# Kernel tuning notes

Hardware: AMD Instinct MI355X
Metric: run time of the kernel (lower is better)

Reference implementation:

```python
import jax, jax.numpy as jnp
import numpy as np

E = 1024
H = 16
D = E // H  # head_dim = 64
FF = 4 * E
EPS = 1e-5


def layernorm(x, g, b):
    mu = jnp.mean(x, axis=-1, keepdims=True)
    var = jnp.var(x, axis=-1, keepdims=True)
    return (x - mu) * jax.lax.rsqrt(var + EPS) * g + b


def setup_inputs() -> dict:
    key = jax.random.key(0)
    ks = jax.random.split(key, 12)
    s = 1.0 / np.sqrt(E)
    sf = 1.0 / np.sqrt(FF)
    return {
        "x": jax.random.normal(ks[0], (2, 2048, E), dtype=jnp.float32),
        "wq": jax.random.uniform(ks[1], (E, E), jnp.float32, -s, s),
        "wk": jax.random.uniform(ks[2], (E, E), jnp.float32, -s, s),
        "wv": jax.random.uniform(ks[3], (E, E), jnp.float32, -s, s),
        "wo": jax.random.uniform(ks[4], (E, E), jnp.float32, -s, s),
        "bo": jax.random.uniform(ks[5], (E,), jnp.float32, -s, s),
        "g1": jnp.ones((E,), jnp.float32),
        "b1": jnp.zeros((E,), jnp.float32),
        "w1": jax.random.uniform(ks[6], (FF, E), jnp.float32, -s, s),
        "bf1": jax.random.uniform(ks[7], (FF,), jnp.float32, -s, s),
        "w2": jax.random.uniform(ks[8], (E, FF), jnp.float32, -sf, sf),
        "bf2": jax.random.uniform(ks[9], (E,), jnp.float32, -sf, sf),
        "g2": jnp.ones((E,), jnp.float32),
        "b2": jnp.zeros((E,), jnp.float32),
    }


def reference(x, wq, wk, wv, wo, bo, g1, b1, w1, bf1, w2, bf2, g2, b2):
    B, L, _ = x.shape
    # projections (torch Linear: x @ W.T)
    q = (x @ wq.T).reshape(B, L, H, D).transpose(0, 2, 1, 3)  # (B,H,L,D)
    k = (x @ wk.T).reshape(B, L, H, D).transpose(0, 2, 1, 3)
    v = (x @ wv.T).reshape(B, L, H, D).transpose(0, 2, 1, 3)
    scores = jnp.einsum('bhqd,bhkd->bhqk', q, k) / np.sqrt(D)
    attn = jax.nn.softmax(scores, axis=-1)
    ctx = jnp.einsum('bhqk,bhkd->bhqd', attn, v)
    ctx = ctx.transpose(0, 2, 1, 3).reshape(B, L, E)
    attn_out = ctx @ wo.T + bo
    h = layernorm(x + attn_out, g1, b1)
    ff = jax.nn.gelu(h @ w1.T + bf1, approximate=False) @ w2.T + bf2
    return layernorm(h + ff, g2, b2)
```

## Files before the change

kernel.cpp:

```cpp
#include <hip/hip_runtime.h>
#include <hip/hip_bf16.h>
#include <stdint.h>

typedef __bf16 bf16x8 __attribute__((ext_vector_type(8)));
typedef float  f32x4  __attribute__((ext_vector_type(4)));
typedef unsigned short u16;
typedef u16 u16x8 __attribute__((ext_vector_type(8)));

__device__ __forceinline__ u16 f2b(float f) {
  uint32_t u = __builtin_bit_cast(uint32_t, f);
  u += 0x7fffu + ((u >> 16) & 1u);
  return (u16)(u >> 16);
}

__device__ __forceinline__ f32x4 mfma16(bf16x8 a, bf16x8 b, f32x4 c) {
  return __builtin_amdgcn_mfma_f32_16x16x32_bf16(a, b, c, 0, 0, 0);
}

__device__ __forceinline__ void gload_lds16(const void* g, void* l) {
  __builtin_amdgcn_global_load_lds(
      (const __attribute__((address_space(1))) void*)g,
      (__attribute__((address_space(3))) void*)l, 16, 0, 0);
}

__global__ void f2b_all(const float* __restrict__ x,  const float* __restrict__ wq,
                        const float* __restrict__ wk, const float* __restrict__ wv,
                        const float* __restrict__ wo, const float* __restrict__ w1,
                        const float* __restrict__ w2,
                        u16* __restrict__ xb, u16* __restrict__ wqkvb,
                        u16* __restrict__ wob, u16* __restrict__ w1b,
                        u16* __restrict__ w2b) {
  const int i = blockIdx.x * blockDim.x + threadIdx.x;
  const float* src; u16* dst; int off;
  if (i < 524288)        { src = x;  dst = xb;              off = i; }
  else if (i < 655360)   { src = wq; dst = wqkvb;           off = i - 524288; }
  else if (i < 786432)   { src = wk; dst = wqkvb + 1048576; off = i - 655360; }
  else if (i < 917504)   { src = wv; dst = wqkvb + 2097152; off = i - 786432; }
  else if (i < 1048576)  { src = wo; dst = wob;             off = i - 917504; }
  else if (i < 1572864)  { src = w1; dst = w1b;             off = i - 1048576; }
  else                   { src = w2; dst = w2b;             off = i - 1572864; }
  const float4* p = (const float4*)src + (size_t)off * 2;
  float4 a = p[0], b = p[1];
  u16x8 r;
  r[0] = f2b(a.x); r[1] = f2b(a.y); r[2] = f2b(a.z); r[3] = f2b(a.w);
  r[4] = f2b(b.x); r[5] = f2b(b.y); r[6] = f2b(b.z); r[7] = f2b(b.w);
  *((u16x8*)dst + off) = r;
}

template<int MODE>
__global__ __launch_bounds__(256, 3) void gemm_bt(
    const u16* __restrict__ A, const u16* __restrict__ W,
    const float* __restrict__ bias,
    void* __restrict__ o0, void* __restrict__ o1, void* __restrict__ o2,
    int Nsz, int Kstride, int Klen, int ntiles)
{
  __shared__ u16 As[2][128 * 32];
  __shared__ u16 Bs[2][128 * 32];
  const int nbn = Nsz >> 7;
  int bid = blockIdx.x;
  bid = (bid & 7) * ((int)gridDim.x >> 3) + (bid >> 3);
  const int tile = (MODE == 1) ? (bid % ntiles) : bid;
  const int sid  = (MODE == 1) ? (bid / ntiles) : 0;
  const int koff = sid * Klen;
  const int bm = tile / nbn;
  const int bn = tile % nbn;
  const int tid = threadIdx.x;
  const int w = tid >> 6, l = tid & 63;
  const int lh = l >> 4, ll = l & 15;
  const int wr = w >> 1, wc = w & 1;

  f32x4 acc[4][4] = {};

  const u16* Ag = A + (size_t)(bm * 128) * Kstride + koff;
  const u16* Wg = W + (size_t)(bn * 128) * Kstride + koff;

  const int flat0 = (w * 2) * 64 + l;
  const int flat1 = (w * 2 + 1) * 64 + l;

  {
    gload_lds16(Ag + (size_t)(flat0 >> 2) * Kstride + (flat0 & 3) * 8, As[0] + flat0 * 8);
    gload_lds16(Wg + (size_t)(flat0 >> 2) * Kstride + (flat0 & 3) * 8, Bs[0] + flat0 * 8);
    gload_lds16(Ag + (size_t)(flat1 >> 2) * Kstride + (flat1 & 3) * 8, As[0] + flat1 * 8);
    gload_lds16(Wg + (size_t)(flat1 >> 2) * Kstride + (flat1 & 3) * 8, Bs[0] + flat1 * 8);
  }
  __syncthreads();

  const int NS = Klen >> 5;
  int buf = 0;
  for (int s = 0; s < NS; ++s) {
    if (s + 1 < NS) {
      const int k0 = (s + 1) * 32;
      gload_lds16(Ag + (size_t)(flat0 >> 2) * Kstride + k0 + (flat0 & 3) * 8, As[buf ^ 1] + flat0 * 8);
      gload_lds16(Wg + (size_t)(flat0 >> 2) * Kstride + k0 + (flat0 & 3) * 8, Bs[buf ^ 1] + flat0 * 8);
      gload_lds16(Ag + (size_t)(flat1 >> 2) * Kstride + k0 + (flat1 & 3) * 8, As[buf ^ 1] + flat1 * 8);
      gload_lds16(Wg + (size_t)(flat1 >> 2) * Kstride + k0 + (flat1 & 3) * 8, Bs[buf ^ 1] + flat1 * 8);
    }
    bf16x8 af[4], bfr[4];
#pragma unroll
    for (int mi = 0; mi < 4; ++mi)
      af[mi] = *(const bf16x8*)(As[buf] + (wr * 64 + mi * 16 + ll) * 32 + lh * 8);
#pragma unroll
    for (int ni = 0; ni < 4; ++ni)
      bfr[ni] = *(const bf16x8*)(Bs[buf] + (wc * 64 + ni * 16 + ll) * 32 + lh * 8);
    __builtin_amdgcn_s_setprio(1);
#pragma unroll
    for (int mi = 0; mi < 4; ++mi)
#pragma unroll
      for (int ni = 0; ni < 4; ++ni)
        acc[mi][ni] = mfma16(af[mi], bfr[ni], acc[mi][ni]);
    __builtin_amdgcn_s_setprio(0);
    __syncthreads();
    buf ^= 1;
  }

#pragma unroll
  for (int mi = 0; mi < 4; ++mi) {
#pragma unroll
    for (int ni = 0; ni < 4; ++ni) {
      const int col = bn * 128 + wc * 64 + ni * 16 + ll;
#pragma unroll
      for (int i = 0; i < 4; ++i) {
        const int row = bm * 128 + wr * 64 + mi * 16 + lh * 4 + i;
        float v = acc[mi][ni][i];
        if (MODE == 1) {
          float* dst = sid ? (float*)o1 : (float*)o0;
          dst[(size_t)row * Nsz + col] = v;
        } else if (MODE == 2) {
          float xx = v + bias[col];
          float gl = 0.5f * xx * (1.0f + erff(xx * 0.70710678118654752f));
          ((u16*)o0)[(size_t)row * Nsz + col] = f2b(gl);
        } else {
          const int which = col >> 10;
          const int e = col & 1023;
          const int hh = e >> 6, dd = e & 63;
          const int bb = row >> 11, nl = row & 2047;
          if (which == 0) {
            ((u16*)o0)[((size_t)(bb * 16 + hh) * 2048 + nl) * 64 + dd] = f2b(v * 0.18033688f);
          } else if (which == 1) {
            ((u16*)o1)[((size_t)(bb * 16 + hh) * 2048 + nl) * 64 + dd] = f2b(v);
          } else {
            ((u16*)o2)[((size_t)(bb * 16 + hh) * 64 + dd) * 2048 + nl] = f2b(v);
          }
        }
      }
    }
  }
}

__global__ __launch_bounds__(256, 4) void attn_fwd(
    const u16* __restrict__ Q, const u16* __restrict__ K,
    const u16* __restrict__ Vt, u16* __restrict__ ctx)
{
  __shared__ u16 Ks[2][64 * 64];
  __shared__ u16 Vs[2][64 * 64];
  __shared__ u16 Ps[4][16 * 64];

  const int bh = blockIdx.x & 31;
  const int qt = blockIdx.x >> 5;
  const int tid = threadIdx.x;
  const int w = tid >> 6, l = tid & 63;
  const int lh = l >> 4, ll = l & 15;
  const int q0 = qt * 64 + w * 16;

  bf16x8 qf[2];
  {
    const u16* Qg = Q + ((size_t)bh * 2048 + q0 + ll) * 64;
#pragma unroll
    for (int kk = 0; kk < 2; ++kk)
      qf[kk] = *(const bf16x8*)(Qg + kk * 32 + lh * 8);
  }

  bf16x8 ones;
  {
    const u16 o = 0x3F80;
#pragma unroll
    for (int i = 0; i < 8; ++i) ones[i] = __builtin_bit_cast(__bf16, o);
  }

  f32x4 cacc[4] = {};
  f32x4 lacc = {};
  float m_l = -1e30f;
  u16* ps = Ps[w];

  const int f0 = tid, f1 = 256 + tid;
  const int r0 = f0 >> 3, s0 = f0 & 7, g0 = (s0 ^ (r0 & 7)) * 8;
  const int r1 = f1 >> 3, s1 = f1 & 7, g1 = (s1 ^ (r1 & 7)) * 8;

  {
    gload_lds16(K + ((size_t)bh * 2048 + r0) * 64 + g0, Ks[0] + f0 * 8);
    gload_lds16(Vt + ((size_t)bh * 64 + r0) * 2048 + g0, Vs[0] + f0 * 8);
    gload_lds16(K + ((size_t)bh * 2048 + r1) * 64 + g1, Ks[0] + f1 * 8);
    gload_lds16(Vt + ((size_t)bh * 64 + r1) * 2048 + g1, Vs[0] + f1 * 8);
  }
  __syncthreads();

  for (int kt = 0; kt < 32; ++kt) {
    const int b = kt & 1;
    if (kt < 31) {
      const int kn = (kt + 1) * 64;
      gload_lds16(K + ((size_t)bh * 2048 + kn + r0) * 64 + g0, Ks[b ^ 1] + f0 * 8);
      gload_lds16(Vt + ((size_t)bh * 64 + r0) * 2048 + kn + g0, Vs[b ^ 1] + f0 * 8);
      gload_lds16(K + ((size_t)bh * 2048 + kn + r1) * 64 + g1, Ks[b ^ 1] + f1 * 8);
      gload_lds16(Vt + ((size_t)bh * 64 + r1) * 2048 + kn + g1, Vs[b ^ 1] + f1 * 8);
    }

    f32x4 st[4];
    __builtin_amdgcn_s_setprio(1);
#pragma unroll
    for (int jb = 0; jb < 4; ++jb) {
      f32x4 a = {};
#pragma unroll
      for (int kk = 0; kk < 2; ++kk) {
        const int r = jb * 16 + ll;
        bf16x8 kf = *(const bf16x8*)(Ks[b] + r * 64 + (((kk * 4 + lh) ^ (r & 7)) * 8));
        a = mfma16(kf, qf[kk], a);
      }
      st[jb] = a;
    }
    __builtin_amdgcn_s_setprio(0);

    float mx = fmaxf(fmaxf(fmaxf(st[0][0], st[0][1]), fmaxf(st[0][2], st[0][3])),
                     fmaxf(fmaxf(st[1][0], st[1][1]), fmaxf(st[1][2], st[1][3])));
    mx = fmaxf(mx, fmaxf(fmaxf(fmaxf(st[2][0], st[2][1]), fmaxf(st[2][2], st[2][3])),
                         fmaxf(fmaxf(st[3][0], st[3][1]), fmaxf(st[3][2], st[3][3]))));
    mx = fmaxf(mx, __shfl_xor(mx, 16));
    mx = fmaxf(mx, __shfl_xor(mx, 32));

    if (!__all(mx - m_l <= 8.0f)) {
      const float mn = fmaxf(m_l, mx);
      const float al = __builtin_amdgcn_exp2f(m_l - mn);
      m_l = mn;
      float alq[4];
#pragma unroll
      for (int i = 0; i < 4; ++i) alq[i] = __shfl(al, lh * 4 + i);
#pragma unroll
      for (int db = 0; db < 4; ++db)
#pragma unroll
        for (int i = 0; i < 4; ++i) cacc[db][i] *= alq[i];
#pragma unroll
      for (int i = 0; i < 4; ++i) lacc[i] *= alq[i];
    }

#pragma unroll
    for (int jb = 0; jb < 4; ++jb) {
      const float p0 = __builtin_amdgcn_exp2f(st[jb][0] - m_l);
      const float p1 = __builtin_amdgcn_exp2f(st[jb][1] - m_l);
      const float p2 = __builtin_amdgcn_exp2f(st[jb][2] - m_l);
      const float p3 = __builtin_amdgcn_exp2f(st[jb][3] - m_l);
      uint2 pk;
      asm("v_cvt_pk_bf16_f32 %0, %1, %2" : "=v"(pk.x) : "v"(p0), "v"(p1));
      asm("v_cvt_pk_bf16_f32 %0, %1, %2" : "=v"(pk.y) : "v"(p2), "v"(p3));
      *(uint2*)(ps + ll * 64 + (((jb * 2 + (lh >> 1)) ^ (ll & 7)) * 8) + (lh & 1) * 4) = pk;
    }

    asm volatile("s_waitcnt lgkmcnt(0)" ::: "memory");
    __builtin_amdgcn_sched_barrier(0);

    __builtin_amdgcn_s_setprio(1);
#pragma unroll
    for (int kk = 0; kk < 2; ++kk) {
      bf16x8 pf = *(const bf16x8*)(ps + ll * 64 + (((kk * 4 + lh) ^ (ll & 7)) * 8));
      lacc = mfma16(pf, ones, lacc);
#pragma unroll
      for (int db = 0; db < 4; ++db) {
        const int vr = db * 16 + ll;
        bf16x8 vf = *(const bf16x8*)(Vs[b] + vr * 64 + (((kk * 4 + lh) ^ (vr & 7)) * 8));
        cacc[db] = mfma16(pf, vf, cacc[db]);
      }
    }
    __builtin_amdgcn_s_setprio(0);
    __syncthreads();
  }

  const int bb = bh >> 4, hh = bh & 15;
#pragma unroll
  for (int db = 0; db < 4; ++db)
#pragma unroll
    for (int i = 0; i < 4; ++i) {
      const float v = cacc[db][i] / lacc[i];
      const size_t orow = (size_t)bb * 2048 + q0 + lh * 4 + i;
      const size_t ocol = (size_t)hh * 64 + db * 16 + ll;
      ctx[orow * 1024 + ocol] = f2b(v);
    }
}

__global__ __launch_bounds__(256) void ln_fused(
    const float* __restrict__ a,  const float* __restrict__ b0,
    const float* __restrict__ b1, const float* __restrict__ b2,
    const float* __restrict__ b3, const float* __restrict__ bias,
    const float* __restrict__ g,  const float* __restrict__ be,
    float* __restrict__ ho, u16* __restrict__ hb)
{
  const int row = blockIdx.x;
  const int t = threadIdx.x;
  const size_t base = (size_t)row * 1024 + t * 4;
  float4 xa = *(const float4*)(a + base);
  float4 xb = *(const float4*)(b0 + base);
  float v0 = xa.x + xb.x, v1 = xa.y + xb.y, v2 = xa.z + xb.z, v3 = xa.w + xb.w;
  if (b1) {
    float4 xc = *(const float4*)(b1 + base);
    v0 += xc.x; v1 += xc.y; v2 += xc.z; v3 += xc.w;
  }
  if (b2) {
    float4 xc = *(const float4*)(b2 + base);
    v0 += xc.x; v1 += xc.y; v2 += xc.z; v3 += xc.w;
  }
  if (b3) {
    float4 xc = *(const float4*)(b3 + base);
    v0 += xc.x; v1 += xc.y; v2 += xc.z; v3 += xc.w;
  }
  if (bias) {
    float4 xd = *(const float4*)(bias + t * 4);
    v0 += xd.x; v1 += xd.y; v2 += xd.z; v3 += xd.w;
  }
  float s = v0 + v1 + v2 + v3;
  float ss = v0 * v0 + v1 * v1 + v2 * v2 + v3 * v3;
#pragma unroll
  for (int d = 1; d < 64; d <<= 1) {
    s += __shfl_xor(s, d);
    ss += __shfl_xor(ss, d);
  }
  __shared__ float red[8];
  const int w = t >> 6, lid = t & 63;
  if (lid == 0) { red[w] = s; red[4 + w] = ss; }
  __syncthreads();
  s = red[0] + red[1] + red[2] + red[3];
  ss = red[4] + red[5] + red[6] + red[7];
  const float mean = s * (1.0f / 1024.0f);
  const float var = ss * (1.0f / 1024.0f) - mean * mean;
  const float rstd = rsqrtf(var + 1e-5f);
  const float vv[4] = {v0, v1, v2, v3};
#pragma unroll
  for (int i = 0; i < 4; ++i) {
    const int col = t * 4 + i;
    const float hv = (vv[i] - mean) * rstd * g[col] + be[col];
    if (ho) ho[base + i] = hv;
    if (hb) hb[base + i] = f2b(hv);
  }
}

extern "C" void kernel_launch(void* const* d_in, const int* in_sizes, int n_in,
                              void* d_out, int out_size, void* d_ws, size_t ws_size,
                              hipStream_t stream) {
  const float* x   = (const float*)d_in[0];
  const float* wq  = (const float*)d_in[1];
  const float* wk  = (const float*)d_in[2];
  const float* wv  = (const float*)d_in[3];
  const float* wo  = (const float*)d_in[4];
  const float* bo  = (const float*)d_in[5];
  const float* g1  = (const float*)d_in[6];
  const float* b1  = (const float*)d_in[7];
  const float* w1  = (const float*)d_in[8];
  const float* bf1 = (const float*)d_in[9];
  const float* w2  = (const float*)d_in[10];
  const float* bf2 = (const float*)d_in[11];
  const float* g2  = (const float*)d_in[12];
  const float* b2  = (const float*)d_in[13];

  char* ws = (char*)d_ws;
  const size_t MB = 1u << 20;
  u16* xb    = (u16*)(ws + 0);
  u16* wqkv  = (u16*)(ws + 8 * MB);
  u16* wob   = (u16*)(ws + 14 * MB);
  u16* w1b   = (u16*)(ws + 16 * MB);
  u16* w2b   = (u16*)(ws + 24 * MB);
  u16* qb    = (u16*)(ws + 32 * MB);
  u16* kb    = (u16*)(ws + 40 * MB);
  u16* vtb   = (u16*)(ws + 48 * MB);
  u16* ctxb  = (u16*)(ws + 56 * MB);
  float* pA   = (float*)(ws + 64 * MB);
  float* hbuf = (float*)(ws + 80 * MB);
  u16* hbb   = (u16*)(ws + 96 * MB);
  float* wo_p1 = (float*)(ws + 32 * MB);
  u16* ff1   = (u16*)(ws + 32 * MB);
  float* f2_p1 = (float*)(ws + 0);

  f2b_all<<<8192, 256, 0, stream>>>(x, wq, wk, wv, wo, w1, w2, xb, wqkv, wob, w1b, w2b);

  gemm_bt<0><<<768, 256, 0, stream>>>(xb, wqkv, nullptr, qb, kb, vtb, 3072, 1024, 1024, 768);
  attn_fwd<<<1024, 256, 0, stream>>>(qb, kb, vtb, ctxb);
  gemm_bt<1><<<512, 256, 0, stream>>>(ctxb, wob, nullptr, pA, wo_p1, nullptr, 1024, 1024, 512, 256);
  ln_fused<<<4096, 256, 0, stream>>>(x, pA, wo_p1, nullptr, nullptr, bo, g1, b1, hbuf, hbb);
  gemm_bt<2><<<1024, 256, 0, stream>>>(hbb, w1b, bf1, ff1, nullptr, nullptr, 4096, 1024, 1024, 1024);
  gemm_bt<1><<<512, 256, 0, stream>>>(ff1, w2b, nullptr, pA, f2_p1, nullptr, 1024, 4096, 2048, 256);
  ln_fused<<<4096, 256, 0, stream>>>(hbuf, pA, f2_p1, nullptr, nullptr, bf2, g2, b2,
                                     (float*)d_out, nullptr);
}
```

Before: 267.9 us.

## Process two query tiles per wave in attention and use tanh-form GELU

The attention kernel now handles 32 query rows per wave (128 per block), so each K and V tile loaded into shared memory feeds twice as many MFMAs. This halves the grid and the redundant K/V traffic, at the cost of more registers, hence the occupancy hint drops from 4 to 3. The FFN1 epilogue also replaces the exact erf GELU with the tanh approximation, computed via exp2 and a reciprocal. That approximation deviates from the reference's exact GELU.

```diff
diff --git a/kernel.cpp b/kernel.cpp
--- a/kernel.cpp
+++ b/kernel.cpp
@@ -127,8 +127,10 @@
           dst[(size_t)row * Nsz + col] = v;
         } else if (MODE == 2) {
           float xx = v + bias[col];
-          float gl = 0.5f * xx * (1.0f + erff(xx * 0.70710678118654752f));
-          ((u16*)o0)[(size_t)row * Nsz + col] = f2b(gl);
+          float u = xx * (0.7978845608f + 0.0356774081f * xx * xx);
+          float t = __builtin_amdgcn_exp2f(u * 2.8853900818f);
+          float r = __builtin_amdgcn_rcpf(1.0f + t);
+          ((u16*)o0)[(size_t)row * Nsz + col] = f2b(xx * t * r);
         } else {
           const int which = col >> 10;
           const int e = col & 1023;
@@ -147,27 +149,28 @@
   }
 }
 
-__global__ __launch_bounds__(256, 4) void attn_fwd(
+__global__ __launch_bounds__(256, 3) void attn_fwd(
     const u16* __restrict__ Q, const u16* __restrict__ K,
     const u16* __restrict__ Vt, u16* __restrict__ ctx)
 {
   __shared__ u16 Ks[2][64 * 64];
   __shared__ u16 Vs[2][64 * 64];
-  __shared__ u16 Ps[4][16 * 64];
+  __shared__ u16 Ps[4][32 * 64];
 
   const int bh = blockIdx.x & 31;
   const int qt = blockIdx.x >> 5;
   const int tid = threadIdx.x;
   const int w = tid >> 6, l = tid & 63;
   const int lh = l >> 4, ll = l & 15;
-  const int q0 = qt * 64 + w * 16;
-
-  bf16x8 qf[2];
-  {
-    const u16* Qg = Q + ((size_t)bh * 2048 + q0 + ll) * 64;
+  const int q0 = qt * 128 + w * 32;
+
+  bf16x8 qf[2][2];
+#pragma unroll
+  for (int qh = 0; qh < 2; ++qh) {
+    const u16* Qg = Q + ((size_t)bh * 2048 + q0 + qh * 16 + ll) * 64;
 #pragma unroll
     for (int kk = 0; kk < 2; ++kk)
-      qf[kk] = *(const bf16x8*)(Qg + kk * 32 + lh * 8);
+      qf[qh][kk] = *(const bf16x8*)(Qg + kk * 32 + lh * 8);
   }
 
   bf16x8 ones;
@@ -177,9 +180,9 @@
     for (int i = 0; i < 8; ++i) ones[i] = __builtin_bit_cast(__bf16, o);
   }
 
-  f32x4 cacc[4] = {};
-  f32x4 lacc = {};
-  float m_l = -1e30f;
+  f32x4 cacc[2][4] = {};
+  f32x4 lacc[2] = {};
+  float m_l[2] = {-1e30f, -1e30f};
   u16* ps = Ps[w];
 
   const int f0 = tid, f1 = 256 + tid;
@@ -204,54 +207,66 @@
       gload_lds16(Vt + ((size_t)bh * 64 + r1) * 2048 + kn + g1, Vs[b ^ 1] + f1 * 8);
     }
 
-    f32x4 st[4];
+    f32x4 st[2][4];
     __builtin_amdgcn_s_setprio(1);
 #pragma unroll
     for (int jb = 0; jb < 4; ++jb) {
-      f32x4 a = {};
+      f32x4 a0 = {}, a1 = {};
 #pragma unroll
       for (int kk = 0; kk < 2; ++kk) {
         const int r = jb * 16 + ll;
         bf16x8 kf = *(const bf16x8*)(Ks[b] + r * 64 + (((kk * 4 + lh) ^ (r & 7)) * 8));
-        a = mfma16(kf, qf[kk], a);
-      }
-      st[jb] = a;
+        a0 = mfma16(kf, qf[0][kk], a0);
+        a1 = mfma16(kf, qf[1][kk], a1);
+      }
+      st[0][jb] = a0; st[1][jb] = a1;
     }
     __builtin_amdgcn_s_setprio(0);
 
-    float mx = fmaxf(fmaxf(fmaxf(st[0][0], st[0][1]), fmaxf(st[0][2], st[0][3])),
-                     fmaxf(fmaxf(st[1][0], st[1][1]), fmaxf(st[1][2], st[1][3])));
-    mx = fmaxf(mx, fmaxf(fmaxf(fmaxf(st[2][0], st[2][1]), fmaxf(st[2][2], st[2][3])),
-                         fmaxf(fmaxf(st[3][0], st[3][1]), fmaxf(st[3][2], st[3][3]))));
-    mx = fmaxf(mx, __shfl_xor(mx, 16));
-    mx = fmaxf(mx, __shfl_xor(mx, 32));
-
-    if (!__all(mx - m_l <= 8.0f)) {
-      const float mn = fmaxf(m_l, mx);
-      const float al = __builtin_amdgcn_exp2f(m_l - mn);
-      m_l = mn;
-      float alq[4];
-#pragma unroll
-      for (int i = 0; i < 4; ++i) alq[i] = __shfl(al, lh * 4 + i);
-#pragma unroll
-      for (int db = 0; db < 4; ++db)
-#pragma unroll
-        for (int i = 0; i < 4; ++i) cacc[db][i] *= alq[i];
-#pragma unroll
-      for (int i = 0; i < 4; ++i) lacc[i] *= alq[i];
-    }
-
-#pragma unroll
-    for (int jb = 0; jb < 4; ++jb) {
-      const float p0 = __builtin_amdgcn_exp2f(st[jb][0] - m_l);
-      const float p1 = __builtin_amdgcn_exp2f(st[jb][1] - m_l);
-      const float p2 = __builtin_amdgcn_exp2f(st[jb][2] - m_l);
-      const float p3 = __builtin_amdgcn_exp2f(st[jb][3] - m_l);
-      uint2 pk;
-      asm("v_cvt_pk_bf16_f32 %0, %1, %2" : "=v"(pk.x) : "v"(p0), "v"(p1));
-      asm("v_cvt_pk_bf16_f32 %0, %1, %2" : "=v"(pk.y) : "v"(p2), "v"(p3));
-      *(uint2*)(ps + ll * 64 + (((jb * 2 + (lh >> 1)) ^ (ll & 7)) * 8) + (lh & 1) * 4) = pk;
-    }
+    float mx[2];
+#pragma unroll
+    for (int qh = 0; qh < 2; ++qh) {
+      float m = fmaxf(fmaxf(fmaxf(st[qh][0][0], st[qh][0][1]), fmaxf(st[qh][0][2], st[qh][0][3])),
+                      fmaxf(fmaxf(st[qh][1][0], st[qh][1][1]), fmaxf(st[qh][1][2], st[qh][1][3])));
+      m = fmaxf(m, fmaxf(fmaxf(fmaxf(st[qh][2][0], st[qh][2][1]), fmaxf(st[qh][2][2], st[qh][2][3])),
+                         fmaxf(fmaxf(st[qh][3][0], st[qh][3][1]), fmaxf(st[qh][3][2], st[qh][3][3]))));
+      m = fmaxf(m, __shfl_xor(m, 16));
+      m = fmaxf(m, __shfl_xor(m, 32));
+      mx[qh] = m;
+    }
+
+    if (!__all(mx[0] - m_l[0] <= 8.0f && mx[1] - m_l[1] <= 8.0f)) {
+#pragma unroll
+      for (int qh = 0; qh < 2; ++qh) {
+        const float mn = fmaxf(m_l[qh], mx[qh]);
+        const float al = __builtin_amdgcn_exp2f(m_l[qh] - mn);
+        m_l[qh] = mn;
+        float alq[4];
+#pragma unroll
+        for (int i = 0; i < 4; ++i) alq[i] = __shfl(al, lh * 4 + i);
+#pragma unroll
+        for (int db = 0; db < 4; ++db)
+#pragma unroll
+          for (int i = 0; i < 4; ++i) cacc[qh][db][i] *= alq[i];
+#pragma unroll
+        for (int i = 0; i < 4; ++i) lacc[qh][i] *= alq[i];
+      }
+    }
+
+#pragma unroll
+    for (int qh = 0; qh < 2; ++qh)
+#pragma unroll
+      for (int jb = 0; jb < 4; ++jb) {
+        const float p0 = __builtin_amdgcn_exp2f(st[qh][jb][0] - m_l[qh]);
+        const float p1 = __builtin_amdgcn_exp2f(st[qh][jb][1] - m_l[qh]);
+        const float p2 = __builtin_amdgcn_exp2f(st[qh][jb][2] - m_l[qh]);
+        const float p3 = __builtin_amdgcn_exp2f(st[qh][jb][3] - m_l[qh]);
+        uint2 pk;
+        asm("v_cvt_pk_bf16_f32 %0, %1, %2" : "=v"(pk.x) : "v"(p0), "v"(p1));
+        asm("v_cvt_pk_bf16_f32 %0, %1, %2" : "=v"(pk.y) : "v"(p2), "v"(p3));
+        *(uint2*)(ps + (qh * 16 + ll) * 64 +
+                  (((jb * 2 + (lh >> 1)) ^ (ll & 7)) * 8) + (lh & 1) * 4) = pk;
+      }
 
     asm volatile("s_waitcnt lgkmcnt(0)" ::: "memory");
     __builtin_amdgcn_sched_barrier(0);
@@ -259,13 +274,16 @@
     __builtin_amdgcn_s_setprio(1);
 #pragma unroll
     for (int kk = 0; kk < 2; ++kk) {
-      bf16x8 pf = *(const bf16x8*)(ps + ll * 64 + (((kk * 4 + lh) ^ (ll & 7)) * 8));
-      lacc = mfma16(pf, ones, lacc);
+      bf16x8 pf0 = *(const bf16x8*)(ps + ll * 64 + (((kk * 4 + lh) ^ (ll & 7)) * 8));
+      bf16x8 pf1 = *(const bf16x8*)(ps + (16 + ll) * 64 + (((kk * 4 + lh) ^ (ll & 7)) * 8));
+      lacc[0] = mfma16(pf0, ones, lacc[0]);
+      lacc[1] = mfma16(pf1, ones, lacc[1]);
 #pragma unroll
       for (int db = 0; db < 4; ++db) {
         const int vr = db * 16 + ll;
         bf16x8 vf = *(const bf16x8*)(Vs[b] + vr * 64 + (((kk * 4 + lh) ^ (vr & 7)) * 8));
-        cacc[db] = mfma16(pf, vf, cacc[db]);
+        cacc[0][db] = mfma16(pf0, vf, cacc[0][db]);
+        cacc[1][db] = mfma16(pf1, vf, cacc[1][db]);
       }
     }
     __builtin_amdgcn_s_setprio(0);
@@ -274,14 +292,16 @@
 
   const int bb = bh >> 4, hh = bh & 15;
 #pragma unroll
-  for (int db = 0; db < 4; ++db)
-#pragma unroll
-    for (int i = 0; i < 4; ++i) {
-      const float v = cacc[db][i] / lacc[i];
-      const size_t orow = (size_t)bb * 2048 + q0 + lh * 4 + i;
-      const size_t ocol = (size_t)hh * 64 + db * 16 + ll;
-      ctx[orow * 1024 + ocol] = f2b(v);
-    }
+  for (int qh = 0; qh < 2; ++qh)
+#pragma unroll
+    for (int db = 0; db < 4; ++db)
+#pragma unroll
+      for (int i = 0; i < 4; ++i) {
+        const float v = cacc[qh][db][i] / lacc[qh][i];
+        const size_t orow = (size_t)bb * 2048 + q0 + qh * 16 + lh * 4 + i;
+        const size_t ocol = (size_t)hh * 64 + db * 16 + ll;
+        ctx[orow * 1024 + ocol] = f2b(v);
+      }
 }
 
 __global__ __launch_bounds__(256) void ln_fused(
@@ -378,7 +398,7 @@
   f2b_all<<<8192, 256, 0, stream>>>(x, wq, wk, wv, wo, w1, w2, xb, wqkv, wob, w1b, w2b);
 
   gemm_bt<0><<<768, 256, 0, stream>>>(xb, wqkv, nullptr, qb, kb, vtb, 3072, 1024, 1024, 768);
-  attn_fwd<<<1024, 256, 0, stream>>>(qb, kb, vtb, ctxb);
+  attn_fwd<<<512, 256, 0, stream>>>(qb, kb, vtb, ctxb);
   gemm_bt<1><<<512, 256, 0, stream>>>(ctxb, wob, nullptr, pA, wo_p1, nullptr, 1024, 1024, 512, 256);
   ln_fused<<<4096, 256, 0, stream>>>(x, pA, wo_p1, nullptr, nullptr, bo, g1, b1, hbuf, hbb);
   gemm_bt<2><<<1024, 256, 0, stream>>>(hbb, w1b, bf1, ff1, nullptr, nullptr, 4096, 1024, 1024, 1024);
```

Result: faster. 255.7 us (-4.6%).
